# Optimization experiments

Measured on AMD Instinct MI355X. Metric: run time of the kernel, lower is better.

Reference implementation:

```python
import jax, jax.numpy as jnp
import numpy as np

SEQ_LEN, BATCH, FEAT, HID, NUM_LAYERS = 256, 128, 512, 1024, 3


def setup_inputs() -> dict:
    key = jax.random.key(0)
    ks = jax.random.split(key, 9)
    s = 0.02
    x = jax.random.normal(ks[0], (SEQ_LEN, BATCH, FEAT), dtype=jnp.float32)
    # layer 0 cell: input size FEAT; layers 1..L-1: input size HID
    W_ih0 = jax.random.normal(ks[1], (4 * HID, FEAT), dtype=jnp.float32) * s
    W_ih_rest = jax.random.normal(ks[2], (NUM_LAYERS - 1, 4 * HID, HID), dtype=jnp.float32) * s
    W_hh = jax.random.normal(ks[3], (NUM_LAYERS, 4 * HID, HID), dtype=jnp.float32) * s
    b_ih = jax.random.normal(ks[4], (NUM_LAYERS, 4 * HID), dtype=jnp.float32) * s
    b_hh = jax.random.normal(ks[5], (NUM_LAYERS, 4 * HID), dtype=jnp.float32) * s
    W_out = jax.random.normal(ks[6], (HID, HID), dtype=jnp.float32) * s
    b_out = jax.random.normal(ks[7], (HID,), dtype=jnp.float32) * s
    return {"x": x, "W_ih0": W_ih0, "W_ih_rest": W_ih_rest, "W_hh": W_hh,
            "b_ih": b_ih, "b_hh": b_hh, "W_out": W_out, "b_out": b_out}


def _lstm_cell(inp, h, c, W_ih, W_hh, b):
    # torch nn.LSTMCell: gates = inp@W_ih^T + h@W_hh^T + b_ih + b_hh
    gates = inp @ W_ih.T + h @ W_hh.T + b  # [B, 4H]
    i, f, g, o = jnp.split(gates, 4, axis=-1)
    c_new = jax.nn.sigmoid(f) * c + jax.nn.sigmoid(i) * jnp.tanh(g)
    h_new = jax.nn.sigmoid(o) * jnp.tanh(c_new)
    return h_new, c_new


def reference(x, W_ih0, W_ih_rest, W_hh, b_ih, b_hh, W_out, b_out):
    L = W_hh.shape[0]
    B = x.shape[1]
    H = W_hh.shape[-1]
    b = b_ih + b_hh  # [L, 4H]

    def step(carry, xt):
        h, c = carry  # each [L, B, H]
        h0, c0 = _lstm_cell(xt, h[0], c[0], W_ih0, W_hh[0], b[0])
        ft = h0 @ W_out.T + b_out
        hs, cs = [h0], [c0]
        for j in range(1, L):
            hj, cj = _lstm_cell(ft, h[j], c[j], W_ih_rest[j - 1], W_hh[j], b[j])
            ft = (hj + ft) @ W_out.T + b_out  # residual + shared Linear
            hs.append(hj)
            cs.append(cj)
        return (jnp.stack(hs), jnp.stack(cs)), ft

    h0 = jnp.zeros((L, B, H), dtype=x.dtype)
    c0 = jnp.zeros((L, B, H), dtype=x.dtype)
    _, out = jax.lax.scan(step, (h0, c0), x)
    return out  # [seq_len, batch, hidden]
```

## Files before the change

### kernel.cpp

```cpp
#include <hip/hip_runtime.h>
#include <cmath>

#define SEQ  256
#define BATCH 128
#define FEAT 512
#define HID  1024
#define G4   4096
#define BH (BATCH*HID)

typedef __attribute__((ext_vector_type(8))) _Float16 f16x8;
typedef __attribute__((ext_vector_type(4))) float f32x4;
typedef __attribute__((ext_vector_type(4))) unsigned u32x4;

__device__ __forceinline__ unsigned short f16_rne(float f) {
  _Float16 h = (_Float16)f;
  return __builtin_bit_cast(unsigned short, h);
}
__device__ __forceinline__ float f16_tof(unsigned short s) {
  return (float)__builtin_bit_cast(_Float16, s);
}
__device__ __forceinline__ void gload16(const unsigned short* g, unsigned short* l) {
  __builtin_amdgcn_global_load_lds(
      (const __attribute__((address_space(1))) unsigned int*)g,
      (__attribute__((address_space(3))) unsigned int*)l, 16, 0, 0);
}
__device__ __forceinline__ float sigf(float x) { return 1.f/(1.f+expf(-x)); }

__device__ __forceinline__ void st1u(unsigned* p, unsigned v) {
  asm volatile("global_store_dword %0, %1, off sc0 sc1" :: "v"(p), "v"(v) : "memory");
}
__device__ __forceinline__ u32x4 ld4u(const unsigned* p) {
  u32x4 r;
  asm volatile("global_load_dwordx4 %0, %1, off sc0 sc1" : "=v"(r) : "v"(p) : "memory");
  return r;
}
__device__ __forceinline__ unsigned ld1u(const unsigned* p) {
  unsigned r;
  asm volatile("global_load_dword %0, %1, off sc0 sc1" : "=v"(r) : "v"(p) : "memory");
  return r;
}
__device__ __forceinline__ void wait0() {
  asm volatile("s_waitcnt vmcnt(0)" ::: "memory");
  __builtin_amdgcn_sched_barrier(0);
}
__device__ __forceinline__ unsigned ldcnt(unsigned* p) {
  return __hip_atomic_load(p, __ATOMIC_RELAXED, __HIP_MEMORY_SCOPE_SYSTEM);
}
__device__ __forceinline__ void bump(unsigned* p) {
  __hip_atomic_fetch_add(p, 1u, __ATOMIC_RELAXED, __HIP_MEMORY_SCOPE_SYSTEM);
}


__global__ __launch_bounds__(256)
void conv16(const float* __restrict__ src, unsigned short* __restrict__ dst, int n4) {
  for (int i = blockIdx.x*256 + threadIdx.x; i < n4; i += gridDim.x*256) {
    const float4 v = ((const float4*)src)[i];
    ushort4 h;
    h.x = f16_rne(v.x); h.y = f16_rne(v.y); h.z = f16_rne(v.z); h.w = f16_rne(v.w);
    ((ushort4*)dst)[i] = h;
  }
}

__global__ __launch_bounds__(256)
void transp16(const float* __restrict__ src, unsigned short* __restrict__ dst) {
  const int i = blockIdx.x*256 + threadIdx.x;
  const int k = i >> 10, c = i & 1023;
  dst[(c << 10) + k] = f16_rne(src[i]);
}

__global__ __launch_bounds__(256)
void conv_perm16(const float* __restrict__ src, unsigned short* __restrict__ dst,
                 int n4, int ksh) {
  for (int i = blockIdx.x*256 + threadIdx.x; i < n4; i += gridDim.x*256) {
    const float4 v = ((const float4*)src)[i];
    const int row = i >> ksh, cq = i & ((1 << ksh) - 1);
    const int prow = ((row & 1023) << 2) | (row >> 10);
    ushort4 h;
    h.x = f16_rne(v.x); h.y = f16_rne(v.y); h.z = f16_rne(v.z); h.w = f16_rne(v.w);
    ((ushort4*)dst)[(prow << ksh) + cq] = h;
  }
}

__global__ __launch_bounds__(256)
void bias_perm(const float* __restrict__ bih, const float* __restrict__ bhh,
               float* __restrict__ bperm) {
  const int i = blockIdx.x*256 + threadIdx.x;
  if (i >= 3*G4) return;
  const int l = i >> 12, r = i & 4095;
  const int prow = ((r & 1023) << 2) | (r >> 10);
  bperm[(l << 12) + prow] = bih[i] + bhh[i];
}

__global__ __launch_bounds__(256)
void gemvf(const float* __restrict__ W, const float* __restrict__ b,
           float* __restrict__ dst, int nrows) {
  const int r = blockIdx.x*256 + threadIdx.x;
  if (r >= nrows) return;
  const float4* wr = (const float4*)(W + (size_t)r*HID);
  float acc = 0.f;
  for (int k = 0; k < 256; ++k) {
    const float4 w = wr[k]; const float4 bb = ((const float4*)b)[k];
    acc += w.x*bb.x + w.y*bb.y + w.z*bb.z + w.w*bb.w;
  }
  dst[((r & 1023) << 2) | (r >> 10)] += acc;
}

template<int MI, int NI, int WRN, int WCN>
__device__ __forceinline__ void mm_core(
    unsigned short* lds, int n0, int kstart, int nch,
    const unsigned short* A1, int K1, const unsigned short* A2,
    const unsigned short* W1, const unsigned short* W2,
    f32x4 acc[MI][NI])
{
  constexpr int AROWS = WRN*MI*16;
  constexpr int WROWS = WCN*NI*16;
  constexpr int OW  = AROWS*64;
  constexpr int STRIDE = (AROWS + WROWS)*64;
  constexpr int NLD = (AROWS + WROWS)/64;
  const int tid = threadIdx.x;
  const int lane = tid & 63, wave = tid >> 6;
  const int wr = wave / WCN, wc = wave % WCN;
  const int rl = lane >> 3, cc = lane & 7;
  const int gcol = (cc ^ rl) << 3;

  auto stage = [&](int ch) {
    const int kg = kstart + (ch << 6);
    const unsigned short *pA, *pW; int sA, sW;
    if (kg < K1) { pA = A1 + kg; sA = K1;   pW = W1 + kg; sW = K1; }
    else { const int k2 = kg - K1; pA = A2 + k2; sA = 1024; pW = W2 + k2; sW = 1024; }
    unsigned short* const db = lds + (ch & 1)*STRIDE;
    #pragma unroll
    for (int q = 0; q < NLD; ++q) {
      const int g = wave*NLD + q;
      if (g < AROWS/8)
        gload16(pA + (size_t)(g*8 + rl)*sA + gcol, db + g*512);
      else
        gload16(pW + (size_t)(n0 + (g - AROWS/8)*8 + rl)*sW + gcol, db + g*512);
    }
  };

  stage(0);
  for (int ch = 0; ch < nch; ++ch) {
    if (ch + 1 < nch) {
      stage(ch + 1);
      asm volatile("s_waitcnt vmcnt(6)" ::: "memory");
    } else {
      asm volatile("s_waitcnt vmcnt(0)" ::: "memory");
    }
    __builtin_amdgcn_sched_barrier(0);
    __builtin_amdgcn_s_barrier();
    const unsigned short* const cb = lds + (ch & 1)*STRIDE;
    #pragma unroll
    for (int kh = 0; kh < 2; ++kh) {
      const int j0 = (kh << 2) + (lane >> 4);
      f16x8 ah[MI], bh[NI];
      #pragma unroll
      for (int mi = 0; mi < MI; ++mi) {
        const int row = wr*(MI*16) + (mi << 4) + (lane & 15);
        const int off = row*64 + ((j0 ^ (row & 7)) << 3);
        ah[mi] = *(const f16x8*)(cb + off);
      }
      #pragma unroll
      for (int ni = 0; ni < NI; ++ni) {
        const int wrow = wc*(NI*16) + (ni << 4) + (lane & 15);
        const int off = wrow*64 + ((j0 ^ (wrow & 7)) << 3);
        bh[ni] = *(const f16x8*)(cb + OW + off);
      }
      #pragma unroll
      for (int mi = 0; mi < MI; ++mi)
        #pragma unroll
        for (int ni = 0; ni < NI; ++ni)
          acc[mi][ni] = __builtin_amdgcn_mfma_f32_16x16x32_f16(ah[mi], bh[ni], acc[mi][ni], 0,0,0);
    }
    __builtin_amdgcn_s_barrier();
  }
}

__global__ __launch_bounds__(512, 2)
void wfuse_kernel(const unsigned short* __restrict__ A,
                  const unsigned short* __restrict__ WT,
                  unsigned short* __restrict__ dstP)
{
  __shared__ unsigned short smem[2*(128+256)*64];
  const int mb = blockIdx.x, jy = blockIdx.y;
  const unsigned short* Ar = A + (size_t)(mb*128)*HID;
  f32x4 z4 = {0.f,0.f,0.f,0.f};
  f32x4 acc[4][4];
  #pragma unroll
  for (int a = 0; a < 4; ++a) { acc[a][0]=z4; acc[a][1]=z4; acc[a][2]=z4; acc[a][3]=z4; }
  mm_core<4,4,2,4>(smem, jy << 8, 0, 16, Ar, HID, Ar, WT, WT, acc);

  const int lane = threadIdx.x & 63, wave = threadIdx.x >> 6;
  const int wr = wave >> 2, wc = wave & 3;
  const int rb = (lane >> 4) << 2, cbl = lane & 15;
  #pragma unroll
  for (int mi = 0; mi < 4; ++mi)
    #pragma unroll
    for (int ni = 0; ni < 4; ++ni)
      #pragma unroll
      for (int r = 0; r < 4; ++r) {
        const int row = mb*128 + (wr << 6) + (mi << 4) + rb + r;
        const int col = (jy << 8) + (wc << 6) + (ni << 4) + cbl;
        dstP[((size_t)(((row & 1023) << 2) | (row >> 10)) << 10) + col] = f16_rne(acc[mi][ni][r]);
      }
}

__global__ __launch_bounds__(512, 1)
void diag_fused(int d,
    const unsigned short* __restrict__ xC,
    unsigned short* __restrict__ hC,
    unsigned short* __restrict__ sC,
    const unsigned short* __restrict__ Wih0p, const unsigned short* __restrict__ Whhp,
    const unsigned short* __restrict__ Wf1p,  const unsigned short* __restrict__ Wf2p,
    const unsigned short* __restrict__ WoutC,
    const float* __restrict__ bperm, const float* __restrict__ bout,
    float* __restrict__ cst, unsigned* __restrict__ slabs,
    unsigned* __restrict__ tk, float* __restrict__ out)
{
  __shared__ unsigned short smem[2*(128+256)*64];
  const int bid = blockIdx.x, tid = threadIdx.x;
  const int p = d & 1, rp = 1 - p;

  int l, jt, kz, KZ, gid, role;
  if (bid < 64)       { l=0; jt=bid>>2;            kz=bid&3; KZ=4; gid=jt;    role=0; }
  else if (bid < 128) { l=1; int u=bid-64;  jt=u>>2; kz=u&3; KZ=4; gid=16+jt; role=0; }
  else if (bid < 144) { l=1; int w=bid-128; jt=w>>2; kz=w&3; KZ=4; gid=48+jt; role=1; }
  else if (bid < 208) { l=2; int u=bid-144; jt=u>>2; kz=u&3; KZ=4; gid=32+jt; role=0; }
  else if (bid < 224) { l=2; int w=bid-208; jt=w>>2; kz=w&3; KZ=4; gid=52+jt; role=1; }
  else                { l=3; int u=bid-224; jt=u>>2; kz=u&3; KZ=4; gid=56+jt; role=2; }
  const int t = d - ((role==2) ? 3 : l);
  if (t < 0 || t >= SEQ) return;

  const unsigned short *A1_, *A2_, *W1_, *W2_;
  int K1, kstart, nch;
  if (role == 0) {
    if (l == 0) {
      A1_ = xC + (size_t)t*BATCH*FEAT;
      K1 = FEAT; W1_ = Wih0p; kstart = kz*384; nch = 6;
    } else {
      A1_ = sC + ((size_t)rp*3 + (l-1))*BH;
      K1 = HID; W1_ = (l==1) ? Wf1p : Wf2p; kstart = kz*512; nch = 8;
    }
    A2_ = hC + ((size_t)rp*3 + l)*BH;
    W2_ = Whhp + (size_t)l*G4*HID;
  } else if (role == 1) {
    A1_ = sC + ((size_t)rp*3 + (l-1))*BH;
    K1 = HID; W1_ = WoutC; W2_ = WoutC; A2_ = A1_;
    kstart = kz*256; nch = 4;
  } else {
    A1_ = sC + ((size_t)rp*3 + 2)*BH;
    K1 = HID; W1_ = WoutC; W2_ = WoutC; A2_ = A1_;
    kstart = kz*256; nch = 4;
  }

  f32x4 z4 = {0.f,0.f,0.f,0.f};
  f32x4 acc[4][4];
  #pragma unroll
  for (int a = 0; a < 4; ++a) { acc[a][0]=z4; acc[a][1]=z4; acc[a][2]=z4; acc[a][3]=z4; }
  mm_core<4,4,2,4>(smem, jt << 8, kstart, nch, A1_, K1, A2_, W1_, W2_, acc);

  {
    const int lane = tid & 63, wave = tid >> 6;
    const int wr = wave >> 2, wc = wave & 3;
    const int rb = (lane >> 4) << 2, cbl = lane & 15;
    unsigned* const sb = slabs + (size_t)bid * 16384;
    #pragma unroll
    for (int mi = 0; mi < 4; ++mi)
      #pragma unroll
      for (int ni = 0; ni < 4; ++ni) {
        const int row = (wr << 6) + (mi << 4) + rb;
        const int col = (wc << 6) + (ni << 4) + cbl;
        const unsigned p0 = (unsigned)f16_rne(acc[mi][ni][0])
                          | ((unsigned)f16_rne(acc[mi][ni][1]) << 16);
        const unsigned p1 = (unsigned)f16_rne(acc[mi][ni][2])
                          | ((unsigned)f16_rne(acc[mi][ni][3]) << 16);
        st1u(sb + ((row >> 1) << 8) + col, p0);
        st1u(sb + (((row >> 1) + 1) << 8) + col, p1);
      }
  }
  asm volatile("s_waitcnt vmcnt(0)" ::: "memory");
  __syncthreads();
  if (tid == 0) bump(&tk[gid*32]);
  if (role == 1) return;

  {
    if (tid == 0) {
      unsigned* a = &tk[gid*32];
      const int ta = KZ*(t+1);
      while ((int)ldcnt(a) - ta < 0) __builtin_amdgcn_s_sleep(2);
    } else if (tid == 1 && role == 0 && l) {
      unsigned* b = &tk[((l==1 ? 48 : 52) + (jt >> 2))*32];
      const int tb = 4*(t+1);
      while ((int)ldcnt(b) - tb < 0) __builtin_amdgcn_s_sleep(2);
    }
    __syncthreads();
  }

  const unsigned* gb = slabs + (size_t)(bid - kz) * 16384;
  if (role == 0) {
    const unsigned* eb = l ? slabs + (size_t)((l==1 ? 128 : 208) + ((jt >> 2) << 2)) * 16384
                           : nullptr;
    #pragma unroll
    for (int it = 0; it < 2; ++it) {
      const int u = it*512 + tid;
      const int nl = u & 63, rpl = u >> 6;
      const int rpair = (kz << 4) + rpl;
      const int o = (rpair << 8) + (nl << 2);
      u32x4 a0 = ld4u(gb + o);
      u32x4 a1 = ld4u(gb + 16384 + o);
      u32x4 a2 = ld4u(gb + 32768 + o);
      u32x4 a3 = ld4u(gb + 49152 + o);
      unsigned e0 = 0, e1 = 0, e2 = 0, e3 = 0;
      const int n = (jt << 6) + nl;
      if (l) {
        const int oe = (rpair << 8) + (n & 255);
        e0 = ld1u(eb + oe);
        e1 = ld1u(eb + 16384 + oe);
        e2 = ld1u(eb + 32768 + oe);
        e3 = ld1u(eb + 49152 + oe);
      }
      wait0();
      float gate[4][2];
      #pragma unroll
      for (int g = 0; g < 4; ++g) {
        const unsigned v0 = a0[g], v1 = a1[g], v2 = a2[g], v3 = a3[g];
        gate[g][0] = f16_tof((unsigned short)(v0 & 0xffff)) + f16_tof((unsigned short)(v1 & 0xffff))
                   + f16_tof((unsigned short)(v2 & 0xffff)) + f16_tof((unsigned short)(v3 & 0xffff));
        gate[g][1] = f16_tof((unsigned short)(v0 >> 16)) + f16_tof((unsigned short)(v1 >> 16))
                   + f16_tof((unsigned short)(v2 >> 16)) + f16_tof((unsigned short)(v3 >> 16));
      }
      const float4 bp = ((const float4*)(bperm + (l << 12)))[n];
      float ftv[2] = {0.f, 0.f};
      if (l) {
        const float bo = bout[n];
        ftv[0] = bo + f16_tof((unsigned short)(e0 & 0xffff)) + f16_tof((unsigned short)(e1 & 0xffff))
                    + f16_tof((unsigned short)(e2 & 0xffff)) + f16_tof((unsigned short)(e3 & 0xffff));
        ftv[1] = bo + f16_tof((unsigned short)(e0 >> 16)) + f16_tof((unsigned short)(e1 >> 16))
                    + f16_tof((unsigned short)(e2 >> 16)) + f16_tof((unsigned short)(e3 >> 16));
      }
      #pragma unroll
      for (int j = 0; j < 2; ++j) {
        const int m = (rpair << 1) + j;
        const float gi_ = gate[0][j] + bp.x;
        const float gf_ = gate[1][j] + bp.y;
        const float gg_ = gate[2][j] + bp.z;
        const float go_ = gate[3][j] + bp.w;
        const size_t ci = (size_t)l*BH + (m << 10) + n;
        const float cn = sigf(gf_)*cst[ci] + sigf(gi_)*tanhf(gg_);
        cst[ci] = cn;
        const float h = sigf(go_)*tanhf(cn);
        const size_t wi = ((size_t)p*3 + l)*BH + (m << 10) + n;
        hC[wi] = f16_rne(h);
        sC[wi] = f16_rne(h + (l ? ftv[j] : 0.f));
      }
    }
  } else {
    float* const op = out + (size_t)t*BH;
    #pragma unroll
    for (int it = 0; it < 8; ++it) {
      const int u = it*512 + tid;
      const int col = u & 255, rpl = u >> 8;
      const int rpair = (kz << 4) + rpl;
      const int o = (rpair << 8) + col;
      const unsigned v0 = ld1u(gb + o);
      const unsigned v1 = ld1u(gb + 16384 + o);
      const unsigned v2 = ld1u(gb + 32768 + o);
      const unsigned v3 = ld1u(gb + 49152 + o);
      wait0();
      const int n = (jt << 8) + col;
      const float bo = bout[n];
      const float r0 = bo + f16_tof((unsigned short)(v0 & 0xffff)) + f16_tof((unsigned short)(v1 & 0xffff))
                         + f16_tof((unsigned short)(v2 & 0xffff)) + f16_tof((unsigned short)(v3 & 0xffff));
      const float r1 = bo + f16_tof((unsigned short)(v0 >> 16)) + f16_tof((unsigned short)(v1 >> 16))
                         + f16_tof((unsigned short)(v2 >> 16)) + f16_tof((unsigned short)(v3 >> 16));
      const int m = rpair << 1;
      op[((size_t)m << 10) + n] = r0;
      op[((size_t)(m+1) << 10) + n] = r1;
    }
  }
}


extern "C" void kernel_launch(void* const* d_in, const int* in_sizes, int n_in,
                              void* d_out, int out_size, void* d_ws, size_t ws_size,
                              hipStream_t stream) {
  const float* x    = (const float*)d_in[0];
  const float* Wih0 = (const float*)d_in[1];
  const float* Wihr = (const float*)d_in[2];
  const float* Whh  = (const float*)d_in[3];
  const float* bih  = (const float*)d_in[4];
  const float* bhh  = (const float*)d_in[5];
  const float* Wout = (const float*)d_in[6];
  const float* bout = (const float*)d_in[7];
  float* out = (float*)d_out;

  char* base = (char*)d_ws;
  size_t off = 0;
  auto alloc = [&](size_t bytes) -> char* {
    char* p = base + off;
    off = (off + bytes + 255) & ~(size_t)255;
    return p;
  };
  unsigned* tk = (unsigned*)alloc(64ull*32*4);
  unsigned* slabs = (unsigned*)alloc(240ull*16384*4);
  float* cst   = (float*)alloc(3ull*BH*4);
  float* bperm = (float*)alloc(3ull*G4*4);
  unsigned short* hC = (unsigned short*)alloc(2ull*3*BH*2);
  unsigned short* sC = (unsigned short*)alloc(2ull*3*BH*2);
  unsigned short* xC = (unsigned short*)alloc((size_t)SEQ*BATCH*FEAT*2);
  unsigned short* Wih0p = (unsigned short*)alloc((size_t)G4*FEAT*2);
  unsigned short* Whhp  = (unsigned short*)alloc(3ull*G4*HID*2);
  unsigned short* Wf1p  = (unsigned short*)alloc((size_t)G4*HID*2);
  unsigned short* Wf2p  = (unsigned short*)alloc((size_t)G4*HID*2);
  unsigned short* WoutC = (unsigned short*)alloc((size_t)HID*HID*2);
  unsigned short* WoutT = (unsigned short*)alloc((size_t)HID*HID*2);
  unsigned short* WrC   = (unsigned short*)alloc(2ull*G4*HID*2);

  conv16<<<2048, 256, 0, stream>>>(Wihr, WrC, 2*G4*HID/4);
  conv16<<<1024, 256, 0, stream>>>(Wout, WoutC, HID*HID/4);
  transp16<<<4096, 256, 0, stream>>>(Wout, WoutT);
  conv_perm16<<<2048, 256, 0, stream>>>(Wih0, Wih0p, G4*FEAT/4, 7);
  for (int l = 0; l < 3; ++l)
    conv_perm16<<<2048, 256, 0, stream>>>(Whh + (size_t)l*G4*HID,
        Whhp + (size_t)l*G4*HID, G4*HID/4, 8);
  conv16<<<2048, 256, 0, stream>>>(x, xC, SEQ*BATCH*FEAT/4);
  wfuse_kernel<<<dim3(32,4), 512, 0, stream>>>(WrC,                  WoutT, Wf1p);
  wfuse_kernel<<<dim3(32,4), 512, 0, stream>>>(WrC + (size_t)G4*HID, WoutT, Wf2p);
  bias_perm<<<48, 256, 0, stream>>>(bih, bhh, bperm);
  gemvf<<<16, 256, 0, stream>>>(Wihr,                  bout, bperm + G4,   G4);
  gemvf<<<16, 256, 0, stream>>>(Wihr + (size_t)G4*HID, bout, bperm + 2*G4, G4);

  hipMemsetAsync(cst, 0, 3ull*BH*4, stream);
  hipMemsetAsync(hC, 0, 2ull*3*BH*2, stream);
  hipMemsetAsync(tk, 0, 64ull*32*4, stream);

  for (int d = 0; d < SEQ + 3; ++d) {
    diag_fused<<<240, 512, 0, stream>>>(d, xC, hC, sC,
        Wih0p, Whhp, Wf1p, Wf2p, WoutC, bperm, bout, cst, slabs, tk, out);
  }
}
```

Baseline: 4.668 ms.

## Widen gate-GEMM N-tile to 512 with 8-way K split for LSTM blocks

LSTM gate blocks now compute a 128x512 output tile instead of 128x256, and split K eight ways instead of four. The same 64 blocks per layer therefore cover each gate tile with more partial-sum slabs. The wider tile gives each A-tile load more reuse and shortens each block's K loop. In exchange it doubles LDS and accumulator registers, and the epilogue must reduce 8 partial slabs instead of 4. Slab sizes, ticket indices and the residual-slab indexing are adjusted to match.

```diff
diff --git a/kernel.cpp b/kernel.cpp
--- a/kernel.cpp
+++ b/kernel.cpp
@@ -7,6 +7,7 @@
 #define HID  1024
 #define G4   4096
 #define BH (BATCH*HID)
+#define SLAB 32768
 
 typedef __attribute__((ext_vector_type(8))) _Float16 f16x8;
 typedef __attribute__((ext_vector_type(4))) float f32x4;
@@ -143,7 +144,8 @@
   for (int ch = 0; ch < nch; ++ch) {
     if (ch + 1 < nch) {
       stage(ch + 1);
-      asm volatile("s_waitcnt vmcnt(6)" ::: "memory");
+      if constexpr (NLD == 10) asm volatile("s_waitcnt vmcnt(10)" ::: "memory");
+      else                     asm volatile("s_waitcnt vmcnt(6)" ::: "memory");
     } else {
       asm volatile("s_waitcnt vmcnt(0)" ::: "memory");
     }
@@ -217,53 +219,68 @@
     float* __restrict__ cst, unsigned* __restrict__ slabs,
     unsigned* __restrict__ tk, float* __restrict__ out)
 {
-  __shared__ unsigned short smem[2*(128+256)*64];
+  __shared__ unsigned short smem[2*(128+512)*64];
   const int bid = blockIdx.x, tid = threadIdx.x;
   const int p = d & 1, rp = 1 - p;
 
-  int l, jt, kz, KZ, gid, role;
-  if (bid < 64)       { l=0; jt=bid>>2;            kz=bid&3; KZ=4; gid=jt;    role=0; }
-  else if (bid < 128) { l=1; int u=bid-64;  jt=u>>2; kz=u&3; KZ=4; gid=16+jt; role=0; }
-  else if (bid < 144) { l=1; int w=bid-128; jt=w>>2; kz=w&3; KZ=4; gid=48+jt; role=1; }
-  else if (bid < 208) { l=2; int u=bid-144; jt=u>>2; kz=u&3; KZ=4; gid=32+jt; role=0; }
-  else if (bid < 224) { l=2; int w=bid-208; jt=w>>2; kz=w&3; KZ=4; gid=52+jt; role=1; }
-  else                { l=3; int u=bid-224; jt=u>>2; kz=u&3; KZ=4; gid=56+jt; role=2; }
+  int l, jt, kz, KZ, gid, role, nch, kstart;
+  if (bid < 64)       { l=0; int u=bid;     jt=u>>3; kz=u&7; KZ=8; gid=jt;    role=0; nch=3; kstart=kz*192; }
+  else if (bid < 128) { l=1; int u=bid-64;  jt=u>>3; kz=u&7; KZ=8; gid=8+jt;  role=0; nch=4; kstart=kz*256; }
+  else if (bid < 192) { l=2; int u=bid-128; jt=u>>3; kz=u&7; KZ=8; gid=16+jt; role=0; nch=4; kstart=kz*256; }
+  else if (bid < 208) { l=1; int w=bid-192; jt=w>>2; kz=w&3; KZ=4; gid=48+jt; role=1; nch=4; kstart=kz*256; }
+  else if (bid < 224) { l=2; int w=bid-208; jt=w>>2; kz=w&3; KZ=4; gid=52+jt; role=1; nch=4; kstart=kz*256; }
+  else                { l=3; int u=bid-224; jt=u>>2; kz=u&3; KZ=4; gid=56+jt; role=2; nch=4; kstart=kz*256; }
   const int t = d - ((role==2) ? 3 : l);
   if (t < 0 || t >= SEQ) return;
 
   const unsigned short *A1_, *A2_, *W1_, *W2_;
-  int K1, kstart, nch;
+  int K1;
   if (role == 0) {
     if (l == 0) {
-      A1_ = xC + (size_t)t*BATCH*FEAT;
-      K1 = FEAT; W1_ = Wih0p; kstart = kz*384; nch = 6;
+      A1_ = xC + (size_t)t*BATCH*FEAT; K1 = FEAT; W1_ = Wih0p;
     } else {
-      A1_ = sC + ((size_t)rp*3 + (l-1))*BH;
-      K1 = HID; W1_ = (l==1) ? Wf1p : Wf2p; kstart = kz*512; nch = 8;
+      A1_ = sC + ((size_t)rp*3 + (l-1))*BH; K1 = HID; W1_ = (l==1) ? Wf1p : Wf2p;
     }
     A2_ = hC + ((size_t)rp*3 + l)*BH;
     W2_ = Whhp + (size_t)l*G4*HID;
-  } else if (role == 1) {
-    A1_ = sC + ((size_t)rp*3 + (l-1))*BH;
+  } else {
+    A1_ = sC + ((size_t)rp*3 + ((role==1) ? (l-1) : 2))*BH;
     K1 = HID; W1_ = WoutC; W2_ = WoutC; A2_ = A1_;
-    kstart = kz*256; nch = 4;
+  }
+
+  unsigned* const sb = slabs + (size_t)bid * SLAB;
+  const int lane = tid & 63, wave = tid >> 6;
+  const int rb = (lane >> 4) << 2, cbl = lane & 15;
+
+  if (role == 0) {
+    f32x4 z4 = {0.f,0.f,0.f,0.f};
+    f32x4 acc[4][8];
+    #pragma unroll
+    for (int a = 0; a < 4; ++a)
+      #pragma unroll
+      for (int b = 0; b < 8; ++b) acc[a][b] = z4;
+    mm_core<4,8,2,4>(smem, jt << 9, kstart, nch, A1_, K1, A2_, W1_, W2_, acc);
+    const int wr = wave >> 2, wc = wave & 3;
+    #pragma unroll
+    for (int mi = 0; mi < 4; ++mi)
+      #pragma unroll
+      for (int ni = 0; ni < 8; ++ni) {
+        const int row = (wr << 6) + (mi << 4) + rb;
+        const int col = (wc << 7) + (ni << 4) + cbl;
+        const unsigned p0 = (unsigned)f16_rne(acc[mi][ni][0])
+                          | ((unsigned)f16_rne(acc[mi][ni][1]) << 16);
+        const unsigned p1 = (unsigned)f16_rne(acc[mi][ni][2])
+                          | ((unsigned)f16_rne(acc[mi][ni][3]) << 16);
+        st1u(sb + ((row >> 1) << 9) + col, p0);
+        st1u(sb + (((row >> 1) + 1) << 9) + col, p1);
+      }
   } else {
-    A1_ = sC + ((size_t)rp*3 + 2)*BH;
-    K1 = HID; W1_ = WoutC; W2_ = WoutC; A2_ = A1_;
-    kstart = kz*256; nch = 4;
-  }
-
-  f32x4 z4 = {0.f,0.f,0.f,0.f};
-  f32x4 acc[4][4];
-  #pragma unroll
-  for (int a = 0; a < 4; ++a) { acc[a][0]=z4; acc[a][1]=z4; acc[a][2]=z4; acc[a][3]=z4; }
-  mm_core<4,4,2,4>(smem, jt << 8, kstart, nch, A1_, K1, A2_, W1_, W2_, acc);
-
-  {
-    const int lane = tid & 63, wave = tid >> 6;
+    f32x4 z4 = {0.f,0.f,0.f,0.f};
+    f32x4 acc[4][4];
+    #pragma unroll
+    for (int a = 0; a < 4; ++a) { acc[a][0]=z4; acc[a][1]=z4; acc[a][2]=z4; acc[a][3]=z4; }
+    mm_core<4,4,2,4>(smem, jt << 8, kstart, nch, A1_, K1, A2_, W1_, W2_, acc);
     const int wr = wave >> 2, wc = wave & 3;
-    const int rb = (lane >> 4) << 2, cbl = lane & 15;
-    unsigned* const sb = slabs + (size_t)bid * 16384;
     #pragma unroll
     for (int mi = 0; mi < 4; ++mi)
       #pragma unroll
@@ -289,45 +306,52 @@
       const int ta = KZ*(t+1);
       while ((int)ldcnt(a) - ta < 0) __builtin_amdgcn_s_sleep(2);
     } else if (tid == 1 && role == 0 && l) {
-      unsigned* b = &tk[((l==1 ? 48 : 52) + (jt >> 2))*32];
+      unsigned* b = &tk[((l==1 ? 48 : 52) + (jt >> 1))*32];
       const int tb = 4*(t+1);
       while ((int)ldcnt(b) - tb < 0) __builtin_amdgcn_s_sleep(2);
     }
     __syncthreads();
   }
 
-  const unsigned* gb = slabs + (size_t)(bid - kz) * 16384;
+  const unsigned* gb = slabs + (size_t)(bid - kz) * SLAB;
   if (role == 0) {
-    const unsigned* eb = l ? slabs + (size_t)((l==1 ? 128 : 208) + ((jt >> 2) << 2)) * 16384
+    const unsigned* eb = l ? slabs + (size_t)((l==1 ? 192 : 208) + ((jt >> 1) << 2)) * SLAB
                            : nullptr;
     #pragma unroll
     for (int it = 0; it < 2; ++it) {
       const int u = it*512 + tid;
-      const int nl = u & 63, rpl = u >> 6;
-      const int rpair = (kz << 4) + rpl;
-      const int o = (rpair << 8) + (nl << 2);
+      const int nl = u & 127, rpl = u >> 7;
+      const int rpair = (kz << 3) + rpl;
+      const int o = (rpair << 9) + (nl << 2);
       u32x4 a0 = ld4u(gb + o);
-      u32x4 a1 = ld4u(gb + 16384 + o);
-      u32x4 a2 = ld4u(gb + 32768 + o);
-      u32x4 a3 = ld4u(gb + 49152 + o);
+      u32x4 a1 = ld4u(gb + 1*SLAB + o);
+      u32x4 a2 = ld4u(gb + 2*SLAB + o);
+      u32x4 a3 = ld4u(gb + 3*SLAB + o);
+      u32x4 a4 = ld4u(gb + 4*SLAB + o);
+      u32x4 a5 = ld4u(gb + 5*SLAB + o);
+      u32x4 a6 = ld4u(gb + 6*SLAB + o);
+      u32x4 a7 = ld4u(gb + 7*SLAB + o);
       unsigned e0 = 0, e1 = 0, e2 = 0, e3 = 0;
-      const int n = (jt << 6) + nl;
+      const int n = (jt << 7) + nl;
       if (l) {
         const int oe = (rpair << 8) + (n & 255);
         e0 = ld1u(eb + oe);
-        e1 = ld1u(eb + 16384 + oe);
-        e2 = ld1u(eb + 32768 + oe);
-        e3 = ld1u(eb + 49152 + oe);
+        e1 = ld1u(eb + 1*SLAB + oe);
+        e2 = ld1u(eb + 2*SLAB + oe);
+        e3 = ld1u(eb + 3*SLAB + oe);
       }
       wait0();
       float gate[4][2];
       #pragma unroll
       for (int g = 0; g < 4; ++g) {
-        const unsigned v0 = a0[g], v1 = a1[g], v2 = a2[g], v3 = a3[g];
-        gate[g][0] = f16_tof((unsigned short)(v0 & 0xffff)) + f16_tof((unsigned short)(v1 & 0xffff))
-                   + f16_tof((unsigned short)(v2 & 0xffff)) + f16_tof((unsigned short)(v3 & 0xffff));
-        gate[g][1] = f16_tof((unsigned short)(v0 >> 16)) + f16_tof((unsigned short)(v1 >> 16))
-                   + f16_tof((unsigned short)(v2 >> 16)) + f16_tof((unsigned short)(v3 >> 16));
+        gate[g][0] = f16_tof((unsigned short)(a0[g] & 0xffff)) + f16_tof((unsigned short)(a1[g] & 0xffff))
+                   + f16_tof((unsigned short)(a2[g] & 0xffff)) + f16_tof((unsigned short)(a3[g] & 0xffff))
+                   + f16_tof((unsigned short)(a4[g] & 0xffff)) + f16_tof((unsigned short)(a5[g] & 0xffff))
+                   + f16_tof((unsigned short)(a6[g] & 0xffff)) + f16_tof((unsigned short)(a7[g] & 0xffff));
+        gate[g][1] = f16_tof((unsigned short)(a0[g] >> 16)) + f16_tof((unsigned short)(a1[g] >> 16))
+                   + f16_tof((unsigned short)(a2[g] >> 16)) + f16_tof((unsigned short)(a3[g] >> 16))
+                   + f16_tof((unsigned short)(a4[g] >> 16)) + f16_tof((unsigned short)(a5[g] >> 16))
+                   + f16_tof((unsigned short)(a6[g] >> 16)) + f16_tof((unsigned short)(a7[g] >> 16));
       }
       const float4 bp = ((const float4*)(bperm + (l << 12)))[n];
       float ftv[2] = {0.f, 0.f};
@@ -363,9 +387,9 @@
       const int rpair = (kz << 4) + rpl;
       const int o = (rpair << 8) + col;
       const unsigned v0 = ld1u(gb + o);
-      const unsigned v1 = ld1u(gb + 16384 + o);
-      const unsigned v2 = ld1u(gb + 32768 + o);
-      const unsigned v3 = ld1u(gb + 49152 + o);
+      const unsigned v1 = ld1u(gb + 1*SLAB + o);
+      const unsigned v2 = ld1u(gb + 2*SLAB + o);
+      const unsigned v3 = ld1u(gb + 3*SLAB + o);
       wait0();
       const int n = (jt << 8) + col;
       const float bo = bout[n];
@@ -402,7 +426,7 @@
     return p;
   };
   unsigned* tk = (unsigned*)alloc(64ull*32*4);
-  unsigned* slabs = (unsigned*)alloc(240ull*16384*4);
+  unsigned* slabs = (unsigned*)alloc(240ull*SLAB*4);
   float* cst   = (float*)alloc(3ull*BH*4);
   float* bperm = (float*)alloc(3ull*G4*4);
   unsigned short* hC = (unsigned short*)alloc(2ull*3*BH*2);
```

After: 5.521 ms. 18.3% more time.
